# Optimization experiments

Hardware: AMD Instinct MI355X
Metric: run time of the kernel (lower is better)

The kernel has to match this reference:

```python
import jax, jax.numpy as jnp
import numpy as np

H, D_MODEL, D_K, D_V = 16, 1024, 64, 64
B, L = 2, 2048


def setup_inputs() -> dict:
    key = jax.random.key(0)
    ks = jax.random.split(key, 9)
    s = 1.0 / np.sqrt(D_MODEL)
    return {
        "Q": jax.random.normal(ks[0], (B, L, D_MODEL), jnp.float32),
        "K": jax.random.normal(ks[1], (B, L, D_MODEL), jnp.float32),
        "V": jax.random.normal(ks[2], (B, L, D_MODEL), jnp.float32),
        "mask": jax.random.randint(ks[3], (B, L), 0, 2, jnp.int32),
        "W_Q": jax.random.uniform(ks[4], (D_MODEL, H * D_K), jnp.float32, -s, s),
        "b_Q": jax.random.uniform(ks[5], (H * D_K,), jnp.float32, -s, s),
        "W_K": jax.random.uniform(ks[6], (D_MODEL, H * D_K), jnp.float32, -s, s),
        "W_V": jax.random.uniform(ks[7], (D_MODEL, H * D_V), jnp.float32, -s, s),
        "b_V": jax.random.uniform(ks[8], (H * D_V,), jnp.float32, -s, s),
    }


def reference(Q, K, V, mask, W_Q, b_Q, W_K, W_V, b_V):
    b, lq, _ = Q.shape
    lk = K.shape[1]
    scale = jnp.sqrt(jnp.float32(D_K))
    # projections -> [b, h, len, d]
    q = (Q @ W_Q + b_Q).reshape(b, lq, H, D_K).transpose(0, 2, 1, 3)
    k = (K @ W_K).reshape(b, lk, H, D_K).transpose(0, 2, 1, 3)
    v = (V @ W_V + b_V).reshape(b, lk, H, D_V).transpose(0, 2, 1, 3)
    # scores [b*h, lq, lk]
    A = jnp.einsum("bhqd,bhkd->bhqk", q, k).reshape(b * H, lq, lk) / scale
    # faithful to torch: mask.repeat(h, len_k).view(b*h, -1, len_k)
    mask_rep = jnp.tile(mask, (H, lk)).reshape(b * H, -1, lk)
    A = jnp.where(mask_rep == 0, jnp.float32(-1e9), A)
    alpha = jax.nn.softmax(A, axis=2)
    out = jnp.einsum("bhqk,bhkd->bhqd", alpha.reshape(b, H, lq, lk), v)
    return out.transpose(0, 2, 1, 3).reshape(b, lq, H * D_V)
```

## Files before the change

### kernel.cpp

```cpp
#include <hip/hip_runtime.h>
#include <hip/hip_bf16.h>

typedef float f32x4 __attribute__((ext_vector_type(4)));
typedef short s16x4 __attribute__((ext_vector_type(4)));
typedef unsigned int u32;
typedef unsigned short u16;
typedef unsigned int u32x2 __attribute__((ext_vector_type(2)));
typedef unsigned int u32x4 __attribute__((ext_vector_type(4)));
typedef unsigned short u16x4 __attribute__((ext_vector_type(4)));
typedef unsigned short u16x8 __attribute__((ext_vector_type(8)));

#define MFMA16(a, b, c) __builtin_amdgcn_mfma_f32_16x16x16bf16_1k((a), (b), (c), 0, 0, 0)

#define QSCALE 0.18033688f

__device__ __forceinline__ void mfma32(f32x4& acc, u16x8 a, u16x8 b) {
  asm("v_mfma_f32_16x16x32_bf16 %0, %1, %2, %0" : "+v"(acc) : "v"(a), "v"(b));
}

__device__ __forceinline__ void gload16(const u16* g, u16* l) {
  __builtin_amdgcn_global_load_lds((const __attribute__((address_space(1))) void*)g,
                                   (__attribute__((address_space(3))) void*)l, 16, 0, 0);
}

__device__ __forceinline__ u16 f2bf(float f) {
  u32 u = __builtin_bit_cast(u32, f);
  u += 0x7fffu + ((u >> 16) & 1u);
  return (u16)(u >> 16);
}

__device__ __forceinline__ u32 pk2(float lo, float hi) {
  u32 d;
  asm("v_cvt_pk_bf16_f32 %0, %1, %2" : "=v"(d) : "v"(lo), "v"(hi));
  return d;
}

__device__ __forceinline__ float ex2(float x) {
  float r;
  asm("v_exp_f32 %0, %1" : "=v"(r) : "v"(x));
  return r;
}

__global__ __launch_bounds__(256) void convX(const float* __restrict__ Q, const float* __restrict__ K,
                                             const float* __restrict__ V, u16* __restrict__ o) {
  const int z = blockIdx.y;
  const float* s = z == 0 ? Q : (z == 1 ? K : V);
  const size_t i = ((size_t)blockIdx.x * 256 + threadIdx.x) * 4;
  float4 v4 = *(const float4*)&s[i];
  u16x4 ob = { f2bf(v4.x), f2bf(v4.y), f2bf(v4.z), f2bf(v4.w) };
  *(u16x4*)&o[(size_t)z * 4194304 + i] = ob;
}

__global__ __launch_bounds__(256) void convW(const float* __restrict__ WQ, const float* __restrict__ WK,
                                             const float* __restrict__ WV, u16* __restrict__ o) {
  const int z = blockIdx.z;
  const float* W = z == 0 ? WQ : (z == 1 ? WK : WV);
  const int k0 = blockIdx.x * 8, n = blockIdx.y * 256 + threadIdx.x;
  u16x8 ob;
  #pragma unroll
  for (int j = 0; j < 8; ++j) ob[j] = f2bf(W[(size_t)(k0 + j) * 1024 + n]);
  *(u16x8*)&o[(size_t)z * 1048576 + (size_t)n * 1024 + k0] = ob;
}

__global__ __launch_bounds__(256) void proj_fast(
    const u16* __restrict__ Xb, const u16* __restrict__ Wt,
    const float* __restrict__ bQ, const float* __restrict__ bV, u16* __restrict__ Y0) {
  const int z = blockIdx.z;
  const u16* X = Xb + (size_t)z * 4194304;
  const u16* W = Wt + (size_t)z * 1048576;
  u16* Y = Y0 + (size_t)z * 4194304;
  const float* bias = (z == 0) ? bQ : (z == 1) ? nullptr : bV;
  const float scale = (z == 0) ? QSCALE : 1.0f;

  __shared__ u16 Alds[128][64];
  __shared__ u16 Blds[128][64];

  const int tid = threadIdx.x;
  const int w = tid >> 6, ln = tid & 63, g = ln >> 4, q16 = ln & 15;
  const int x7 = q16 & 7;
  const int wr = w >> 1, wc = w & 1;
  const int rowbase = blockIdx.y * 128, cbase = blockIdx.x * 128;

  const int srow = w * 8 + (ln >> 3);
  const int sch = (ln & 7) ^ ((ln >> 3) & 7);
  const u16* Xg = X + (size_t)(rowbase + srow) * 1024 + sch * 8;
  const u16* Wg = W + (size_t)(cbase + srow) * 1024 + sch * 8;
  u16* Abase = &Alds[0][0] + w * 512;
  u16* Bbase = &Blds[0][0] + w * 512;

  f32x4 acc[4][4] = {};

  for (int k0 = 0; k0 < 1024; k0 += 64) {
    #pragma unroll
    for (int p = 0; p < 4; ++p) {
      gload16(Xg + (size_t)p * 32768 + k0, Abase + p * 2048);
      gload16(Wg + (size_t)p * 32768 + k0, Bbase + p * 2048);
    }
    __syncthreads();

    u16x8 af[4][2], bfr[4][2];
    #pragma unroll
    for (int mi = 0; mi < 4; ++mi)
      #pragma unroll
      for (int ks = 0; ks < 2; ++ks)
        af[mi][ks] = *(const u16x8*)&Alds[wr * 64 + mi * 16 + q16][((ks * 4 + g) ^ x7) * 8];
    #pragma unroll
    for (int ni = 0; ni < 4; ++ni)
      #pragma unroll
      for (int ks = 0; ks < 2; ++ks)
        bfr[ni][ks] = *(const u16x8*)&Blds[wc * 64 + ni * 16 + q16][((ks * 4 + g) ^ x7) * 8];

    #pragma unroll
    for (int mi = 0; mi < 4; ++mi)
      #pragma unroll
      for (int ni = 0; ni < 4; ++ni) {
        mfma32(acc[mi][ni], af[mi][0], bfr[ni][0]);
        mfma32(acc[mi][ni], af[mi][1], bfr[ni][1]);
      }
    __syncthreads();
  }

  #pragma unroll
  for (int ni = 0; ni < 4; ++ni) {
    const int c = cbase + wc * 64 + ni * 16 + q16;
    const float bi = bias ? bias[c] : 0.0f;
    const int hh = c >> 6, d = c & 63;
    #pragma unroll
    for (int mi = 0; mi < 4; ++mi)
      #pragma unroll
      for (int r = 0; r < 4; ++r) {
        const int grow = rowbase + wr * 64 + mi * 16 + g * 4 + r;
        const int bb = grow >> 11, l = grow & 2047;
        const float val = (acc[mi][ni][r] + bi) * scale;
        const size_t idx = (z == 2)
            ? (((size_t)(bb * 16 + hh)) * 64 + d) * 2048 + l
            : (((size_t)(bb * 16 + hh)) * 2048 + l) * 64 + d;
        Y[idx] = f2bf(val);
      }
  }
}

__global__ __launch_bounds__(256) void proj_legacy(
    const float* __restrict__ Qin, const float* __restrict__ Kin, const float* __restrict__ Vin,
    const float* __restrict__ WQ, const float* __restrict__ WK, const float* __restrict__ WV,
    const float* __restrict__ bQ, const float* __restrict__ bV,
    u16* __restrict__ ws) {
  const int z = blockIdx.z;
  const float* X = (z == 0) ? Qin : (z == 1) ? Kin : Vin;
  const float* W = (z == 0) ? WQ : (z == 1) ? WK : WV;
  const float* bias = (z == 0) ? bQ : (z == 1) ? nullptr : bV;
  u16* Y = ws + (size_t)z * 4194304;
  const float scale = (z == 0) ? QSCALE : 1.0f;

  __shared__ u16 Alds[128][40];
  __shared__ u16 Blds[128][40];

  const int tid = threadIdx.x;
  const int w = tid >> 6, ln = tid & 63, g = ln >> 4, q16 = ln & 15;
  const int wr = w >> 1, wc = w & 1;
  const int rowbase = blockIdx.y * 128, cbase = blockIdx.x * 128;

  f32x4 acc[4][4] = {};

  for (int k0 = 0; k0 < 1024; k0 += 32) {
    #pragma unroll
    for (int i = 0; i < 4; ++i) {
      int idx = tid + i * 256;
      int row = idx >> 3, kq = idx & 7;
      const float4 a = *(const float4*)&X[(size_t)(rowbase + row) * 1024 + k0 + kq * 4];
      u16x4 pk = { f2bf(a.x), f2bf(a.y), f2bf(a.z), f2bf(a.w) };
      *(u16x4*)&Alds[row][kq * 4] = pk;
    }
    #pragma unroll
    for (int i = 0; i < 4; ++i) {
      int idx = tid + i * 256;
      int kk = idx >> 5, nq = idx & 31;
      const float4 wv = *(const float4*)&W[(size_t)(k0 + kk) * 1024 + cbase + nq * 4];
      Blds[nq * 4 + 0][kk] = f2bf(wv.x);
      Blds[nq * 4 + 1][kk] = f2bf(wv.y);
      Blds[nq * 4 + 2][kk] = f2bf(wv.z);
      Blds[nq * 4 + 3][kk] = f2bf(wv.w);
    }
    __syncthreads();

    s16x4 af[4][2], bfr[4][2];
    #pragma unroll
    for (int mi = 0; mi < 4; ++mi)
      #pragma unroll
      for (int s = 0; s < 2; ++s)
        af[mi][s] = *(const s16x4*)&Alds[wr * 64 + mi * 16 + q16][s * 16 + g * 4];
    #pragma unroll
    for (int ni = 0; ni < 4; ++ni)
      #pragma unroll
      for (int s = 0; s < 2; ++s)
        bfr[ni][s] = *(const s16x4*)&Blds[wc * 64 + ni * 16 + q16][s * 16 + g * 4];

    #pragma unroll
    for (int mi = 0; mi < 4; ++mi)
      #pragma unroll
      for (int ni = 0; ni < 4; ++ni) {
        acc[mi][ni] = MFMA16(af[mi][0], bfr[ni][0], acc[mi][ni]);
        acc[mi][ni] = MFMA16(af[mi][1], bfr[ni][1], acc[mi][ni]);
      }
    __syncthreads();
  }

  #pragma unroll
  for (int ni = 0; ni < 4; ++ni) {
    const int c = cbase + wc * 64 + ni * 16 + q16;
    const float bi = bias ? bias[c] : 0.0f;
    const int hh = c >> 6, d = c & 63;
    #pragma unroll
    for (int mi = 0; mi < 4; ++mi)
      #pragma unroll
      for (int r = 0; r < 4; ++r) {
        const int grow = rowbase + wr * 64 + mi * 16 + g * 4 + r;
        const int bb = grow >> 11, l = grow & 2047;
        const float val = (acc[mi][ni][r] + bi) * scale;
        const size_t idx = (z == 2)
            ? (((size_t)(bb * 16 + hh)) * 64 + d) * 2048 + l
            : (((size_t)(bb * 16 + hh)) * 2048 + l) * 64 + d;
        Y[idx] = f2bf(val);
      }
  }
}

__global__ __launch_bounds__(256) void attn_kernel(
    const u16* __restrict__ ws, const int* __restrict__ mask, float* __restrict__ out) {
  __shared__ u16 klds[4096];
  __shared__ u16 vtlds[4096];
  __shared__ u16 pt[4][16][72];

  const int bh = blockIdx.y, b = bh >> 4, h = bh & 15;
  const int qbase = blockIdx.x * 64;
  const u16* qp = ws + (size_t)bh * 131072;
  const u16* kp = ws + 4194304 + (size_t)bh * 131072;
  const u16* vp = ws + 8388608 + (size_t)bh * 131072;
  const int* maskrow = mask + (h & 1) * 2048;

  const int tid = threadIdx.x;
  const int w = tid >> 6, ln = tid & 63, g = ln >> 4, q16 = ln & 15;
  const int x7 = q16 & 7;
  const int qrow = qbase + w * 16 + q16;

  u16x8 qf0 = *(const u16x8*)(qp + (size_t)qrow * 64 + g * 8);
  u16x8 qf1 = *(const u16x8*)(qp + (size_t)qrow * 64 + 32 + g * 8);

  const int srow = w * 8 + (ln >> 3);
  const int sch = (ln & 7) ^ (ln >> 3);
  const u16* kg = kp + (size_t)srow * 64 + sch * 8;
  const u16* vg = vp + (size_t)srow * 2048 + sch * 8;

  float l_ = 0.f;
  f32x4 ov[4] = {};

  for (int kt = 0; kt < 2048; kt += 64) {
    __syncthreads();
    gload16(kg + (size_t)kt * 64, klds + w * 512);
    gload16(kg + (size_t)kt * 64 + 2048, klds + w * 512 + 2048);
    gload16(vg + kt, vtlds + w * 512);
    gload16(vg + kt + 65536, vtlds + w * 512 + 2048);
    const unsigned long long bal = __ballot(maskrow[kt + ln] != 0);
    __syncthreads();

    f32x4 sf[4];
    #pragma unroll
    for (int f = 0; f < 4; ++f) {
      u16x8 kf0 = *(const u16x8*)&klds[(f * 16 + q16) * 64 + (g ^ x7) * 8];
      u16x8 kf1 = *(const u16x8*)&klds[(f * 16 + q16) * 64 + ((4 + g) ^ x7) * 8];
      f32x4 s = { 0.f, 0.f, 0.f, 0.f };
      mfma32(s, kf0, qf0);
      mfma32(s, kf1, qf1);
      sf[f] = s;
    }
    {
      const u32 blo = (u32)bal, bhi = (u32)(bal >> 32);
      #pragma unroll
      for (int f = 0; f < 4; ++f) {
        const u32 nib = (((f & 2) ? bhi : blo) >> (16 * (f & 1) + 4 * g)) & 15u;
        #pragma unroll
        for (int r2 = 0; r2 < 4; ++r2)
          if (!((nib >> r2) & 1u)) sf[f][r2] = -1e9f;
      }
    }

    #pragma unroll
    for (int f = 0; f < 4; ++f)
      #pragma unroll
      for (int r2 = 0; r2 < 4; ++r2)
        sf[f][r2] = ex2(sf[f][r2]);
    l_ += ((sf[0][0] + sf[0][1]) + (sf[0][2] + sf[0][3])) +
          ((sf[1][0] + sf[1][1]) + (sf[1][2] + sf[1][3])) +
          ((sf[2][0] + sf[2][1]) + (sf[2][2] + sf[2][3])) +
          ((sf[3][0] + sf[3][1]) + (sf[3][2] + sf[3][3]));

    #pragma unroll
    for (int f = 0; f < 4; ++f) {
      u32x2 pw = { pk2(sf[f][0], sf[f][1]), pk2(sf[f][2], sf[f][3]) };
      *(u16x4*)&pt[w][q16][f * 16 + 4 * g] = __builtin_bit_cast(u16x4, pw);
    }
    asm volatile("s_waitcnt lgkmcnt(0)" ::: "memory");
    u16x8 pa0 = *(const u16x8*)&pt[w][q16][g * 8];
    u16x8 pa1 = *(const u16x8*)&pt[w][q16][32 + g * 8];
    asm volatile("" ::: "memory");

    #pragma unroll
    for (int dc = 0; dc < 4; ++dc) {
      u16x8 vf0 = *(const u16x8*)&vtlds[(dc * 16 + q16) * 64 + (g ^ x7) * 8];
      u16x8 vf1 = *(const u16x8*)&vtlds[(dc * 16 + q16) * 64 + ((4 + g) ^ x7) * 8];
      mfma32(ov[dc], vf0, pa0);
      mfma32(ov[dc], vf1, pa1);
    }
  }

  l_ += __shfl_xor(l_, 16);
  l_ += __shfl_xor(l_, 32);
  const float rinv = 1.0f / l_;
  #pragma unroll
  for (int dc = 0; dc < 4; ++dc) {
    float4 o4 = { ov[dc][0] * rinv, ov[dc][1] * rinv, ov[dc][2] * rinv, ov[dc][3] * rinv };
    *(float4*)&out[((size_t)(b * 2048 + qbase + w * 16 + q16)) * 1024 + h * 64 + dc * 16 + 4 * g] = o4;
  }
}

extern "C" void kernel_launch(void* const* d_in, const int* in_sizes, int n_in,
                              void* d_out, int out_size, void* d_ws, size_t ws_size,
                              hipStream_t stream) {
  const float* Qin = (const float*)d_in[0];
  const float* Kin = (const float*)d_in[1];
  const float* Vin = (const float*)d_in[2];
  const int* mask = (const int*)d_in[3];
  const float* WQ = (const float*)d_in[4];
  const float* bQ = (const float*)d_in[5];
  const float* WK = (const float*)d_in[6];
  const float* WV = (const float*)d_in[7];
  const float* bV = (const float*)d_in[8];
  float* out = (float*)d_out;
  u16* ws = (u16*)d_ws;

  const bool fast = ws_size >= (size_t)56623104;
  if (fast) {
    convX<<<dim3(4096, 3), 256, 0, stream>>>(Qin, Kin, Vin, ws + 12582912);
    convW<<<dim3(128, 4, 3), 256, 0, stream>>>(WQ, WK, WV, ws + 25165824);
    proj_fast<<<dim3(8, 32, 3), 256, 0, stream>>>(ws + 12582912, ws + 25165824, bQ, bV, ws);
  } else {
    proj_legacy<<<dim3(8, 32, 3), 256, 0, stream>>>(Qin, Kin, Vin, WQ, WK, WV, bQ, bV, ws);
  }
  attn_kernel<<<dim3(32, 32), 256, 0, stream>>>(ws, mask, out);
}
```

Measured before the change: 127.4 us.

## Split attention over two key halves and add a combine kernel

Adds a third grid dimension so each attention block handles only half of the key sequence. Each half writes its unnormalized output and row sum to global memory, one into the output buffer and the other into reused workspace. A new combine kernel then adds the two partials and divides by the summed denominators. The aim is more parallel blocks and shorter per-block loops, at the cost of extra global traffic for the partials and one more kernel launch.

```diff
diff --git a/kernel.cpp b/kernel.cpp
--- a/kernel.cpp
+++ b/kernel.cpp
@@ -226,13 +226,19 @@
 }
 
 __global__ __launch_bounds__(256) void attn_kernel(
-    const u16* __restrict__ ws, const int* __restrict__ mask, float* __restrict__ out) {
+    const u16* __restrict__ ws, const int* __restrict__ mask,
+    float* __restrict__ out, float* __restrict__ part1, float* __restrict__ pl) {
   __shared__ u16 klds[4096];
   __shared__ u16 vtlds[4096];
   __shared__ u16 pt[4][16][72];
 
   const int bh = blockIdx.y, b = bh >> 4, h = bh & 15;
   const int qbase = blockIdx.x * 64;
+  const int half = blockIdx.z;
+  const int koff = half << 10;
+  float* po = half ? part1 : out;
+  float* plh = pl + half * 65536;
+
   const u16* qp = ws + (size_t)bh * 131072;
   const u16* kp = ws + 4194304 + (size_t)bh * 131072;
   const u16* vp = ws + 8388608 + (size_t)bh * 131072;
@@ -254,7 +260,7 @@
   float l_ = 0.f;
   f32x4 ov[4] = {};
 
-  for (int kt = 0; kt < 2048; kt += 64) {
+  for (int kt = koff; kt < koff + 1024; kt += 64) {
     __syncthreads();
     gload16(kg + (size_t)kt * 64, klds + w * 512);
     gload16(kg + (size_t)kt * 64 + 2048, klds + w * 512 + 2048);
@@ -315,12 +321,29 @@
 
   l_ += __shfl_xor(l_, 16);
   l_ += __shfl_xor(l_, 32);
-  const float rinv = 1.0f / l_;
+  if ((ln & 48) == 0) plh[bh * 2048 + qrow] = l_;
   #pragma unroll
   for (int dc = 0; dc < 4; ++dc) {
-    float4 o4 = { ov[dc][0] * rinv, ov[dc][1] * rinv, ov[dc][2] * rinv, ov[dc][3] * rinv };
-    *(float4*)&out[((size_t)(b * 2048 + qbase + w * 16 + q16)) * 1024 + h * 64 + dc * 16 + 4 * g] = o4;
-  }
+    float4 o4 = { ov[dc][0], ov[dc][1], ov[dc][2], ov[dc][3] };
+    *(float4*)&po[((size_t)(b * 2048 + qbase + w * 16 + q16)) * 1024 + h * 64 + dc * 16 + 4 * g] = o4;
+  }
+}
+
+__global__ __launch_bounds__(256) void combine_kernel(
+    float* __restrict__ out, const float* __restrict__ part1, const float* __restrict__ pl) {
+  const int e = blockIdx.x * 256 + threadIdx.x;
+  const int i = e * 4;
+  const int b = i >> 21;
+  const int rem = i & 2097151;
+  const int q = rem >> 10;
+  const int c = rem & 1023;
+  const int h = c >> 6;
+  const int bhq = ((b * 16 + h) << 11) + q;
+  const float rinv = 1.0f / (pl[bhq] + pl[65536 + bhq]);
+  float4 a = *(const float4*)&out[i];
+  float4 p = *(const float4*)&part1[i];
+  float4 r = { (a.x + p.x) * rinv, (a.y + p.y) * rinv, (a.z + p.z) * rinv, (a.w + p.w) * rinv };
+  *(float4*)&out[i] = r;
 }
 
 extern "C" void kernel_launch(void* const* d_in, const int* in_sizes, int n_in,
@@ -338,6 +361,9 @@
   float* out = (float*)d_out;
   u16* ws = (u16*)d_ws;
 
+  float* part1 = (float*)(ws + 12582912);
+  float* pl = (float*)(ws + 12582912 + 8388608);
+
   const bool fast = ws_size >= (size_t)56623104;
   if (fast) {
     convX<<<dim3(4096, 3), 256, 0, stream>>>(Qin, Kin, Vin, ws + 12582912);
@@ -346,5 +372,6 @@
   } else {
     proj_legacy<<<dim3(8, 32, 3), 256, 0, stream>>>(Qin, Kin, Vin, WQ, WK, WV, bQ, bV, ws);
   }
-  attn_kernel<<<dim3(32, 32), 256, 0, stream>>>(ws, mask, out);
-}
+  attn_kernel<<<dim3(32, 32, 2), 256, 0, stream>>>(ws, mask, out, part1, pl);
+  combine_kernel<<<4096, 256, 0, stream>>>(out, part1, pl);
+}
```

After: 133.9 us. +5.1%, slower.
